# Kernel tuning notes

Hardware: AMD Instinct MI355X
Metric: run time of the kernel (lower is better)

## Reference

```python
import jax, jax.numpy as jnp
import numpy as np

IN_F = 4096
OUT_F = 4096
B, S = 2, 2048


def setup_inputs() -> dict:
    key = jax.random.key(0)
    k1, k2, k3, k4 = jax.random.split(key, 4)
    input = jax.random.normal(k1, (B, S, IN_F), dtype=jnp.float32)
    int8_weights = jax.random.randint(k2, (OUT_F, IN_F), -128, 128, dtype=jnp.int32).astype(jnp.int8)
    scales = jax.random.normal(k3, (OUT_F,), dtype=jnp.float32)
    bias = jax.random.normal(k4, (1, OUT_F), dtype=jnp.float32)
    return {"input": input, "int8_weights": int8_weights, "scales": scales, "bias": bias}


def reference(input, int8_weights, scales, bias):
    # F.linear(x, W) = x @ W.T ; dequant via per-output-channel scale, then bias
    w = int8_weights.astype(input.dtype)          # [out, in]
    out = jnp.einsum('bsi,oi->bso', input, w)     # [B, S, out]
    out = out * scales + bias                      # broadcast [out] and [1, out]
    return out
```

## Files before the change

kernel.cpp:

```cpp
#include <hip/hip_runtime.h>
#include <hip/hip_bf16.h>

typedef unsigned short u16;
typedef unsigned int u32;
typedef unsigned char u8;
typedef __attribute__((ext_vector_type(4))) int i32x4;

#define MM 4096
#define NN 4096
#define KK 4096

#define BAR __builtin_amdgcn_s_barrier()
#define FENCE asm volatile("" ::: "memory")
#define WAITVM(n) asm volatile("s_waitcnt vmcnt(" #n ")" ::: "memory")

#define ABUF(sh, b) ((sh) + (b) * 32768)
#define BBUF(sh, b) ((sh) + 16384 + (b) * 32768)

__global__ __launch_bounds__(256) void cvt_w_k(const int* __restrict__ w,
                                               u8* __restrict__ o) {
  int i = blockIdx.x * 256 + threadIdx.x;
  const int4* w4 = (const int4*)w + (size_t)i * 4;
  i32x4 r;
#pragma unroll
  for (int j = 0; j < 4; ++j) {
    int4 v = w4[j];
    r[j] = (v.x & 255) | ((v.y & 255) << 8) | ((v.z & 255) << 16) | ((u32)(v.w & 255) << 24);
  }
  *(i32x4*)(o + (size_t)i * 16) = r;
}

__global__ __launch_bounds__(256) void cvt_a_k(const float* __restrict__ x,
                                               u8* __restrict__ o,
                                               float* __restrict__ dA) {
  const int row = blockIdx.x;
  const float4* xr = (const float4*)(x + (size_t)row * KK);
  const int t = threadIdx.x;
  float4 v[4];
  float mx = 0.f;
#pragma unroll
  for (int j = 0; j < 4; ++j) {
    v[j] = xr[t + j * 256];
    mx = fmaxf(mx, fmaxf(fmaxf(fabsf(v[j].x), fabsf(v[j].y)),
                         fmaxf(fabsf(v[j].z), fabsf(v[j].w))));
  }
#pragma unroll
  for (int off = 32; off; off >>= 1) mx = fmaxf(mx, __shfl_down(mx, off));
  __shared__ float sm[4];
  if ((t & 63) == 0) sm[t >> 6] = mx;
  __syncthreads();
  mx = fmaxf(fmaxf(sm[0], sm[1]), fmaxf(sm[2], sm[3]));
  mx = fmaxf(mx, 1e-20f);
  const float inv = 127.0f / mx;
  if (t == 0) dA[row] = mx / 127.0f;
  u32* orow = (u32*)(o + (size_t)row * KK);
#pragma unroll
  for (int j = 0; j < 4; ++j) {
    int qx = (int)rintf(v[j].x * inv), qy = (int)rintf(v[j].y * inv);
    int qz = (int)rintf(v[j].z * inv), qw = (int)rintf(v[j].w * inv);
    orow[t + j * 256] =
        (qx & 255) | ((qy & 255) << 8) | ((qz & 255) << 16) | ((u32)(qw & 255) << 24);
  }
}

__device__ __forceinline__ void gload16(const u8* g, u8* l) {
  __builtin_amdgcn_global_load_lds(
      (const __attribute__((address_space(1))) void*)g,
      (__attribute__((address_space(3))) void*)l, 16, 0, 0);
}

__device__ __forceinline__ void stage_half(const u8* __restrict__ gRowBase,
                                           int k0, u8* ldsHalf, int tid) {
  int row = tid >> 2;
  int c = (tid & 3) ^ ((row >> 1) & 3);
  gload16(gRowBase + (size_t)row * KK + k0 + c * 16, ldsHalf + tid * 16);
}

__device__ __forceinline__ i32x4 ldsfrag(const u8* base, int r, int q) {
  return *(const i32x4*)(base + r * 64 + (((q ^ (r >> 1)) & 3) << 4));
}

#define MFMAI8(a, b, c) __builtin_amdgcn_mfma_i32_16x16x64_i8(a, b, c, 0, 0, 0)

template <int MODE>
__device__ __forceinline__ void do_tile(
    int t, i32x4 (&acc)[8][4], const u8* Ag, const u8* Wg, u8* sh,
    int tid, int lr, int hi, int wr, int wc,
    i32x4 (&afr0)[4], i32x4 (&afr1)[4], i32x4 (&bfr01)[2], i32x4 (&bfr23)[2]) {
  const int b = t & 1;
  u8* Acur = ABUF(sh, b);
  u8* Anxt = ABUF(sh, b ^ 1);
  u8* Bcur = BBUF(sh, b);
  u8* Bnxt = BBUF(sh, b ^ 1);

#pragma unroll
  for (int n = 0; n < 2; ++n)
    bfr23[n] = ldsfrag(Bcur, wc * 64 + (2 + n) * 16 + lr, hi);
  __builtin_amdgcn_s_setprio(1);
#pragma unroll
  for (int m = 0; m < 4; ++m)
#pragma unroll
    for (int n = 0; n < 2; ++n)
      acc[m][n] = MFMAI8(afr0[m], bfr01[n], acc[m][n]);
  __builtin_amdgcn_s_setprio(0);
  FENCE; BAR;

#pragma unroll
  for (int m = 0; m < 4; ++m)
    afr1[m] = ldsfrag(Acur, wr * 128 + 64 + m * 16 + lr, hi);
  if (MODE == 0) {
    stage_half(Wg,            (t + 2) * 64, Bcur,        tid);
    stage_half(Wg + 128 * KK, (t + 2) * 64, Bcur + 8192, tid);
  }
  __builtin_amdgcn_s_setprio(1);
#pragma unroll
  for (int m = 0; m < 4; ++m)
#pragma unroll
    for (int n = 0; n < 2; ++n)
      acc[m][2 + n] = MFMAI8(afr0[m], bfr23[n], acc[m][2 + n]);
  __builtin_amdgcn_s_setprio(0);
  if (MODE == 0) { WAITVM(2); } else if (MODE == 1) { WAITVM(0); }
  FENCE; BAR;

  if (MODE <= 1) {
#pragma unroll
    for (int m = 0; m < 4; ++m)
      afr0[m] = ldsfrag(Anxt, wr * 128 + m * 16 + lr, hi);
  }
  if (MODE == 0) {
    stage_half(Ag,            (t + 2) * 64, Acur,        tid);
    stage_half(Ag + 128 * KK, (t + 2) * 64, Acur + 8192, tid);
  }
  __builtin_amdgcn_s_setprio(1);
#pragma unroll
  for (int m = 0; m < 4; ++m)
#pragma unroll
    for (int n = 0; n < 2; ++n)
      acc[4 + m][n] = MFMAI8(afr1[m], bfr01[n], acc[4 + m][n]);
  __builtin_amdgcn_s_setprio(0);
  FENCE; BAR;

  if (MODE <= 1) {
#pragma unroll
    for (int n = 0; n < 2; ++n)
      bfr01[n] = ldsfrag(Bnxt, wc * 64 + n * 16 + lr, hi);
  }
  __builtin_amdgcn_s_setprio(1);
#pragma unroll
  for (int m = 0; m < 4; ++m)
#pragma unroll
    for (int n = 0; n < 2; ++n)
      acc[4 + m][2 + n] = MFMAI8(afr1[m], bfr23[n], acc[4 + m][2 + n]);
  __builtin_amdgcn_s_setprio(0);
  FENCE; BAR;
}

__global__ __launch_bounds__(512, 2) void gemm_k(const u8* __restrict__ A,
                                                 const u8* __restrict__ W,
                                                 const float* __restrict__ dA,
                                                 const float* __restrict__ scales,
                                                 const float* __restrict__ bias,
                                                 float* __restrict__ out) {
  __shared__ u8 sh[65536];

  const int cpx = gridDim.x >> 3;
  const int wg = (blockIdx.x & 7) * cpx + (blockIdx.x >> 3);
  const int bm = wg >> 4;
  const int bn = wg & 15;

  const int tid = threadIdx.x;
  const int lane = tid & 63;
  const int lr = lane & 15;
  const int hi = lane >> 4;
  const int wid = tid >> 6;
  const int wr = wid >> 2;
  const int wc = wid & 3;

  i32x4 acc[8][4] = {};
  i32x4 afr0[4], afr1[4], bfr01[2], bfr23[2];

  const u8* Ag = A + (size_t)bm * 256 * KK;
  const u8* Wg = W + (size_t)bn * 256 * KK;

  stage_half(Wg,             0, BBUF(sh, 0),        tid);
  stage_half(Wg + 128 * KK,  0, BBUF(sh, 0) + 8192, tid);
  stage_half(Ag,             0, ABUF(sh, 0),        tid);
  stage_half(Ag + 128 * KK,  0, ABUF(sh, 0) + 8192, tid);
  stage_half(Wg,            64, BBUF(sh, 1),        tid);
  stage_half(Wg + 128 * KK, 64, BBUF(sh, 1) + 8192, tid);
  stage_half(Ag,            64, ABUF(sh, 1),        tid);
  stage_half(Ag + 128 * KK, 64, ABUF(sh, 1) + 8192, tid);
  WAITVM(4);
  BAR;
#pragma unroll
  for (int m = 0; m < 4; ++m)
    afr0[m] = ldsfrag(ABUF(sh, 0), wr * 128 + m * 16 + lr, hi);
#pragma unroll
  for (int n = 0; n < 2; ++n)
    bfr01[n] = ldsfrag(BBUF(sh, 0), wc * 64 + n * 16 + lr, hi);

  for (int t = 0; t < 62; ++t)
    do_tile<0>(t, acc, Ag, Wg, sh, tid, lr, hi, wr, wc, afr0, afr1, bfr01, bfr23);
  do_tile<1>(62, acc, Ag, Wg, sh, tid, lr, hi, wr, wc, afr0, afr1, bfr01, bfr23);
  do_tile<2>(63, acc, Ag, Wg, sh, tid, lr, hi, wr, wc, afr0, afr1, bfr01, bfr23);

  const int colb = bn * 256 + wc * 64 + lr;
  const int rowb0 = bm * 256 + wr * 128 + (hi << 2);
#pragma unroll
  for (int m = 0; m < 8; ++m) {
    const int row = rowb0 + m * 16;
    const float da0 = dA[row], da1 = dA[row + 1], da2 = dA[row + 2], da3 = dA[row + 3];
#pragma unroll
    for (int n = 0; n < 4; ++n) {
      const int col = colb + n * 16;
      const float sc = scales[col];
      const float bi = bias[col];
      out[(size_t)(row + 0) * NN + col] = (float)acc[m][n][0] * (da0 * sc) + bi;
      out[(size_t)(row + 1) * NN + col] = (float)acc[m][n][1] * (da1 * sc) + bi;
      out[(size_t)(row + 2) * NN + col] = (float)acc[m][n][2] * (da2 * sc) + bi;
      out[(size_t)(row + 3) * NN + col] = (float)acc[m][n][3] * (da3 * sc) + bi;
    }
  }
}

__global__ __launch_bounds__(256) void fb_k(const float* __restrict__ A,
                                            const int* __restrict__ W,
                                            const float* __restrict__ scales,
                                            const float* __restrict__ bias,
                                            float* __restrict__ out) {
  __shared__ float Arow[KK];
  const int m = blockIdx.y;
  const int n0 = blockIdx.x * 256;
  const int tid = threadIdx.x;
  for (int k = tid; k < KK; k += 256) Arow[k] = A[(size_t)m * KK + k];
  __syncthreads();
  const int n = n0 + tid;
  float acc = 0.f;
  const int* wrp = W + (size_t)n * KK;
  for (int k = 0; k < KK; ++k) acc += Arow[k] * (float)wrp[k];
  out[(size_t)m * NN + n] = acc * scales[n] + bias[n];
}

extern "C" void kernel_launch(void* const* d_in, const int* in_sizes, int n_in,
                              void* d_out, int out_size, void* d_ws, size_t ws_size,
                              hipStream_t stream) {
  const float* input = (const float*)d_in[0];
  const int* w8 = (const int*)d_in[1];
  const float* scales = (const float*)d_in[2];
  const float* bias = (const float*)d_in[3];
  float* out = (float*)d_out;

  const size_t nelem = (size_t)NN * KK;
  const size_t need = 2 * nelem + MM * sizeof(float);

  if (ws_size >= need) {
    u8* Wq = (u8*)d_ws;
    u8* Aq = Wq + nelem;
    float* dA = (float*)(Aq + nelem);
    cvt_w_k<<<4096, 256, 0, stream>>>(w8, Wq);
    cvt_a_k<<<MM, 256, 0, stream>>>(input, Aq, dA);
    gemm_k<<<256, 512, 0, stream>>>(Aq, Wq, dA, scales, bias, out);
  } else {
    dim3 grid(NN / 256, MM);
    fb_k<<<grid, 256, 0, stream>>>(input, w8, scales, bias, out);
  }
}
```

Before: 97.49 us.

## Shrink GEMM tile to 256x128 with 4 waves and 512 blocks

Changes the int8 GEMM block tile from 256x256 with 8 waves to 256x128 with 4 waves, launching 512 blocks of 256 threads and using 48KB of LDS instead of 64KB. Staging is rewritten so each thread issues two 16-byte global-to-LDS loads per 128-row half, and the B buffer is halved. The aim is better CU coverage, since 256 blocks leave the 256 CUs with one block each, and more blocks resident per CU. In exchange each block reuses its A tile across fewer columns, so total global traffic for A doubles.

```diff
diff --git a/kernel.cpp b/kernel.cpp
--- a/kernel.cpp
+++ b/kernel.cpp
@@ -14,8 +14,8 @@
 #define FENCE asm volatile("" ::: "memory")
 #define WAITVM(n) asm volatile("s_waitcnt vmcnt(" #n ")" ::: "memory")
 
-#define ABUF(sh, b) ((sh) + (b) * 32768)
-#define BBUF(sh, b) ((sh) + 16384 + (b) * 32768)
+#define ABUF(sh, b) ((sh) + (b) * 16384)
+#define BBUF(sh, b) ((sh) + 32768 + (b) * 8192)
 
 __global__ __launch_bounds__(256) void cvt_w_k(const int* __restrict__ w,
                                                u8* __restrict__ o) {
@@ -69,11 +69,15 @@
       (__attribute__((address_space(3))) void*)l, 16, 0, 0);
 }
 
-__device__ __forceinline__ void stage_half(const u8* __restrict__ gRowBase,
-                                           int k0, u8* ldsHalf, int tid) {
-  int row = tid >> 2;
-  int c = (tid & 3) ^ ((row >> 1) & 3);
-  gload16(gRowBase + (size_t)row * KK + k0 + c * 16, ldsHalf + tid * 16);
+__device__ __forceinline__ void stage8k(const u8* __restrict__ gRowBase,
+                                        int k0, u8* lds, int tid) {
+#pragma unroll
+  for (int i = 0; i < 2; ++i) {
+    int p = i * 256 + tid;
+    int row = p >> 2;
+    int c = (p & 3) ^ ((row >> 1) & 3);
+    gload16(gRowBase + (size_t)row * KK + k0 + c * 16, lds + p * 16);
+  }
 }
 
 __device__ __forceinline__ i32x4 ldsfrag(const u8* base, int r, int q) {
@@ -108,10 +112,7 @@
 #pragma unroll
   for (int m = 0; m < 4; ++m)
     afr1[m] = ldsfrag(Acur, wr * 128 + 64 + m * 16 + lr, hi);
-  if (MODE == 0) {
-    stage_half(Wg,            (t + 2) * 64, Bcur,        tid);
-    stage_half(Wg + 128 * KK, (t + 2) * 64, Bcur + 8192, tid);
-  }
+  if (MODE == 0) stage8k(Wg, (t + 2) * 64, Bcur, tid);
   __builtin_amdgcn_s_setprio(1);
 #pragma unroll
   for (int m = 0; m < 4; ++m)
@@ -128,8 +129,8 @@
       afr0[m] = ldsfrag(Anxt, wr * 128 + m * 16 + lr, hi);
   }
   if (MODE == 0) {
-    stage_half(Ag,            (t + 2) * 64, Acur,        tid);
-    stage_half(Ag + 128 * KK, (t + 2) * 64, Acur + 8192, tid);
+    stage8k(Ag,            (t + 2) * 64, Acur,        tid);
+    stage8k(Ag + 128 * KK, (t + 2) * 64, Acur + 8192, tid);
   }
   __builtin_amdgcn_s_setprio(1);
 #pragma unroll
@@ -155,42 +156,40 @@
   FENCE; BAR;
 }
 
-__global__ __launch_bounds__(512, 2) void gemm_k(const u8* __restrict__ A,
+__global__ __launch_bounds__(256, 2) void gemm_k(const u8* __restrict__ A,
                                                  const u8* __restrict__ W,
                                                  const float* __restrict__ dA,
                                                  const float* __restrict__ scales,
                                                  const float* __restrict__ bias,
                                                  float* __restrict__ out) {
-  __shared__ u8 sh[65536];
+  __shared__ u8 sh[49152];
 
   const int cpx = gridDim.x >> 3;
   const int wg = (blockIdx.x & 7) * cpx + (blockIdx.x >> 3);
-  const int bm = wg >> 4;
-  const int bn = wg & 15;
+  const int bm = wg >> 5;
+  const int bn = wg & 31;
 
   const int tid = threadIdx.x;
   const int lane = tid & 63;
   const int lr = lane & 15;
   const int hi = lane >> 4;
   const int wid = tid >> 6;
-  const int wr = wid >> 2;
-  const int wc = wid & 3;
+  const int wr = wid >> 1;
+  const int wc = wid & 1;
 
   i32x4 acc[8][4] = {};
   i32x4 afr0[4], afr1[4], bfr01[2], bfr23[2];
 
   const u8* Ag = A + (size_t)bm * 256 * KK;
-  const u8* Wg = W + (size_t)bn * 256 * KK;
-
-  stage_half(Wg,             0, BBUF(sh, 0),        tid);
-  stage_half(Wg + 128 * KK,  0, BBUF(sh, 0) + 8192, tid);
-  stage_half(Ag,             0, ABUF(sh, 0),        tid);
-  stage_half(Ag + 128 * KK,  0, ABUF(sh, 0) + 8192, tid);
-  stage_half(Wg,            64, BBUF(sh, 1),        tid);
-  stage_half(Wg + 128 * KK, 64, BBUF(sh, 1) + 8192, tid);
-  stage_half(Ag,            64, ABUF(sh, 1),        tid);
-  stage_half(Ag + 128 * KK, 64, ABUF(sh, 1) + 8192, tid);
-  WAITVM(4);
+  const u8* Wg = W + (size_t)bn * 128 * KK;
+
+  stage8k(Wg,             0, BBUF(sh, 0),        tid);
+  stage8k(Ag,             0, ABUF(sh, 0),        tid);
+  stage8k(Ag + 128 * KK,  0, ABUF(sh, 0) + 8192, tid);
+  stage8k(Wg,            64, BBUF(sh, 1),        tid);
+  stage8k(Ag,            64, ABUF(sh, 1),        tid);
+  stage8k(Ag + 128 * KK, 64, ABUF(sh, 1) + 8192, tid);
+  WAITVM(6);
   BAR;
 #pragma unroll
   for (int m = 0; m < 4; ++m)
@@ -204,7 +203,7 @@
   do_tile<1>(62, acc, Ag, Wg, sh, tid, lr, hi, wr, wc, afr0, afr1, bfr01, bfr23);
   do_tile<2>(63, acc, Ag, Wg, sh, tid, lr, hi, wr, wc, afr0, afr1, bfr01, bfr23);
 
-  const int colb = bn * 256 + wc * 64 + lr;
+  const int colb = bn * 128 + wc * 64 + lr;
   const int rowb0 = bm * 256 + wr * 128 + (hi << 2);
 #pragma unroll
   for (int m = 0; m < 8; ++m) {
@@ -259,7 +258,7 @@
     float* dA = (float*)(Aq + nelem);
     cvt_w_k<<<4096, 256, 0, stream>>>(w8, Wq);
     cvt_a_k<<<MM, 256, 0, stream>>>(input, Aq, dA);
-    gemm_k<<<256, 512, 0, stream>>>(Aq, Wq, dA, scales, bias, out);
+    gemm_k<<<512, 256, 0, stream>>>(Aq, Wq, dA, scales, bias, out);
   } else {
     dim3 grid(NN / 256, MM);
     fb_k<<<grid, 256, 0, stream>>>(input, w8, scales, bias, out);
```

Result: slower. 101.2 us (median of 2 runs) (+3.8%).
